# Optimization experiments

Hardware: AMD Instinct MI355X
Metric: run time of the kernel (lower is better)

Reference implementation:

```python
import jax, jax.numpy as jnp
import numpy as np

EMBED_DIM = 1024
NUM_HEADS = 16
HEAD_DIM = EMBED_DIM // NUM_HEADS
B, L = 4, 2048


def setup_inputs() -> dict:
    key = jax.random.key(0)
    k1, k2, k3 = jax.random.split(key, 3)
    s = 1.0 / np.sqrt(EMBED_DIM)
    x = jax.random.normal(k1, (B, L, EMBED_DIM), dtype=jnp.float32)
    w_qkv = jax.random.normal(k2, (EMBED_DIM, 3 * EMBED_DIM), dtype=jnp.float32) * s
    b_qkv = jnp.zeros((3 * EMBED_DIM,), dtype=jnp.float32)
    w_out = jax.random.normal(k3, (EMBED_DIM, EMBED_DIM), dtype=jnp.float32) * s
    b_out = jnp.zeros((EMBED_DIM,), dtype=jnp.float32)
    return {"x": x, "w_qkv": w_qkv, "b_qkv": b_qkv, "w_out": w_out, "b_out": b_out}


def reference(x, w_qkv, b_qkv, w_out, b_out):
    Bb, Ll, _ = x.shape
    scale = HEAD_DIM ** -0.5
    qkv = x @ w_qkv + b_qkv                      # [B, L, 3E]
    qkv = qkv.reshape(Bb, Ll, 3, NUM_HEADS, HEAD_DIM)
    q, k, v = qkv[:, :, 0], qkv[:, :, 1], qkv[:, :, 2]   # [B, L, H, D]
    # scores: [B, H, L, L]
    scores = jnp.einsum("bqhd,bkhd->bhqk", q, k) * scale
    causal = jnp.tril(jnp.ones((Ll, Ll), dtype=bool))     # True = keep
    scores = jnp.where(causal, scores, jnp.float32(-1e9))
    attn_probs = jax.nn.softmax(scores, axis=-1)
    context = jnp.einsum("bhqk,bkhd->bqhd", attn_probs, v)
    context = context.reshape(Bb, Ll, EMBED_DIM)
    out = context @ w_out + b_out
    return (out, attn_probs)
```

## Files before the change

kernel.cpp:

```cpp
#include <hip/hip_runtime.h>


typedef __attribute__((ext_vector_type(8))) short short8;
typedef __attribute__((ext_vector_type(4))) float f32x4;

#define MFMA_BF16(a,b,c) __builtin_amdgcn_mfma_f32_16x16x32_bf16((a),(b),(c),0,0,0)

#define GLDS(gp, lp) __builtin_amdgcn_global_load_lds( \
    (const __attribute__((address_space(1))) unsigned int*)(gp), \
    (__attribute__((address_space(3))) unsigned int*)(lp), 16, 0, 0)

__device__ __forceinline__ unsigned short f2bf(float f) {
    union { float f; unsigned u; } v; v.f = f;
    return (unsigned short)((v.u + 0x7FFFu + ((v.u >> 16) & 1u)) >> 16);
}

#define QK_SCALE 0.18033688011112042f

__global__ __launch_bounds__(256) void k_cast(const float* __restrict__ src,
                                              unsigned short* __restrict__ dst, int n8) {
    int i = blockIdx.x * 256 + threadIdx.x;
    if (i >= n8) return;
    const float4* s = (const float4*)src + (size_t)i * 2;
    float4 a = s[0], b = s[1];
    short8 o;
    o[0] = f2bf(a.x); o[1] = f2bf(a.y); o[2] = f2bf(a.z); o[3] = f2bf(a.w);
    o[4] = f2bf(b.x); o[5] = f2bf(b.y); o[6] = f2bf(b.z); o[7] = f2bf(b.w);
    ((short8*)dst)[i] = o;
}

__global__ __launch_bounds__(256) void k_transpose_cast(const float* __restrict__ src,
                                                        unsigned short* __restrict__ dst,
                                                        int R, int C) {
    __shared__ unsigned short t[64][72];
    int c0 = blockIdx.x * 64, r0 = blockIdx.y * 64;
    int tid = threadIdx.x;
    int rl = tid >> 2, cs = (tid & 3) * 16;
    const float* sp = src + (size_t)(r0 + rl) * C + c0 + cs;
    #pragma unroll
    for (int j = 0; j < 16; j += 4) {
        float4 v = *(const float4*)(sp + j);
        t[rl][cs + j + 0] = f2bf(v.x);
        t[rl][cs + j + 1] = f2bf(v.y);
        t[rl][cs + j + 2] = f2bf(v.z);
        t[rl][cs + j + 3] = f2bf(v.w);
    }
    __syncthreads();
    int clq = tid >> 2, rs = (tid & 3) * 16;
    short8 o0, o1;
    #pragma unroll
    for (int j = 0; j < 8; ++j) o0[j] = (short)t[rs + j][clq];
    #pragma unroll
    for (int j = 0; j < 8; ++j) o1[j] = (short)t[rs + 8 + j][clq];
    unsigned short* dp = dst + (size_t)(c0 + clq) * R + r0 + rs;
    *(short8*)dp = o0;
    *(short8*)(dp + 8) = o1;
}

__global__ __launch_bounds__(256) void k_gemm_qkv(
    const unsigned short* __restrict__ A,
    const unsigned short* __restrict__ Bt,
    const float* __restrict__ bias,
    unsigned short* __restrict__ qb,
    unsigned short* __restrict__ kb,
    unsigned short* __restrict__ vb)
{
    __shared__ unsigned short As[128 * 32];
    __shared__ unsigned short Bs[128 * 32];
    const int m0 = blockIdx.y * 128, n0 = blockIdx.x * 128;
    const int tid = threadIdx.x, w = tid >> 6, l = tid & 63;
    const int wm = w >> 1, wn = w & 1;
    const int g = l >> 4, cl = l & 15;
    const int srow = w * 16 + (l >> 2);
    const int soff = (l & 3) * 8;
    f32x4 acc[4][4] = {};

    for (int k0 = 0; k0 < 1024; k0 += 32) {
        __syncthreads();
        #pragma unroll
        for (int c = 0; c < 2; ++c) {
            GLDS(A  + (size_t)(m0 + c * 64 + srow) * 1024 + k0 + soff, &As[(c * 64 + w * 16) * 32]);
            GLDS(Bt + (size_t)(n0 + c * 64 + srow) * 1024 + k0 + soff, &Bs[(c * 64 + w * 16) * 32]);
        }
        __syncthreads();
        short8 af[4], bfr[4];
        #pragma unroll
        for (int i = 0; i < 4; ++i) af[i]  = *(const short8*)&As[(wm * 64 + i * 16 + cl) * 32 + g * 8];
        #pragma unroll
        for (int i = 0; i < 4; ++i) bfr[i] = *(const short8*)&Bs[(wn * 64 + i * 16 + cl) * 32 + g * 8];
        #pragma unroll
        for (int mi = 0; mi < 4; ++mi)
            #pragma unroll
            for (int ni = 0; ni < 4; ++ni)
                acc[mi][ni] = MFMA_BF16(af[mi], bfr[ni], acc[mi][ni]);
    }
    #pragma unroll
    for (int ni = 0; ni < 4; ++ni) {
        int col = n0 + wn * 64 + ni * 16 + cl;
        int which = col >> 10, h = (col >> 6) & 15, d = col & 63;
        unsigned short* dst = which == 0 ? qb : (which == 1 ? kb : vb);
        float bv = bias[col];
        float sc = (which == 0) ? QK_SCALE : 1.0f;
        #pragma unroll
        for (int mi = 0; mi < 4; ++mi) {
            #pragma unroll
            for (int i = 0; i < 4; ++i) {
                int row = m0 + wm * 64 + mi * 16 + g * 4 + i;
                int b = row >> 11, ll = row & 2047;
                dst[((size_t)(b * 16 + h) * 2048 + ll) * 64 + d] = f2bf((acc[mi][ni][i] + bv) * sc);
            }
        }
    }
}

__global__ __launch_bounds__(256) void k_gemm_out(
    const unsigned short* __restrict__ A,
    const unsigned short* __restrict__ Bt,
    const float* __restrict__ bias,
    float* __restrict__ out)
{
    __shared__ unsigned short As[128 * 32];
    __shared__ unsigned short Bs[128 * 32];
    const int m0 = blockIdx.y * 128, n0 = blockIdx.x * 128;
    const int tid = threadIdx.x, w = tid >> 6, l = tid & 63;
    const int wm = w >> 1, wn = w & 1;
    const int g = l >> 4, cl = l & 15;
    const int srow = w * 16 + (l >> 2);
    const int soff = (l & 3) * 8;
    f32x4 acc[4][4] = {};

    for (int k0 = 0; k0 < 1024; k0 += 32) {
        __syncthreads();
        #pragma unroll
        for (int c = 0; c < 2; ++c) {
            GLDS(A  + (size_t)(m0 + c * 64 + srow) * 1024 + k0 + soff, &As[(c * 64 + w * 16) * 32]);
            GLDS(Bt + (size_t)(n0 + c * 64 + srow) * 1024 + k0 + soff, &Bs[(c * 64 + w * 16) * 32]);
        }
        __syncthreads();
        short8 af[4], bfr[4];
        #pragma unroll
        for (int i = 0; i < 4; ++i) af[i]  = *(const short8*)&As[(wm * 64 + i * 16 + cl) * 32 + g * 8];
        #pragma unroll
        for (int i = 0; i < 4; ++i) bfr[i] = *(const short8*)&Bs[(wn * 64 + i * 16 + cl) * 32 + g * 8];
        #pragma unroll
        for (int mi = 0; mi < 4; ++mi)
            #pragma unroll
            for (int ni = 0; ni < 4; ++ni)
                acc[mi][ni] = MFMA_BF16(af[mi], bfr[ni], acc[mi][ni]);
    }
    #pragma unroll
    for (int ni = 0; ni < 4; ++ni) {
        int col = n0 + wn * 64 + ni * 16 + cl;
        float bv = bias[col];
        #pragma unroll
        for (int mi = 0; mi < 4; ++mi) {
            #pragma unroll
            for (int i = 0; i < 4; ++i) {
                int row = m0 + wm * 64 + mi * 16 + g * 4 + i;
                out[(size_t)row * 1024 + col] = acc[mi][ni][i] + bv;
            }
        }
    }
}

__device__ __forceinline__ void stage_qk(const unsigned short* gbase,
                                         unsigned short* lds, int w, int l) {
    const int lr = l >> 3;
    const int lc = (l & 7) ^ lr;
    #pragma unroll
    for (int c = 0; c < 2; ++c) {
        const int r0 = (w * 2 + c) * 8;
        GLDS(gbase + (size_t)(r0 + lr) * 64 + (lc << 3), lds + r0 * 64);
    }
}

__global__ __launch_bounds__(256, 4) void k_attn(
    const unsigned short* __restrict__ qb,
    const unsigned short* __restrict__ kb,
    const unsigned short* __restrict__ vb,
    float* __restrict__ probs,
    unsigned short* __restrict__ ctx)
{
    __shared__ unsigned short Ks[2][64 * 64];
    __shared__ unsigned short Vt[2][64 * 64];
    __shared__ unsigned short Ps[4 * 16 * 64];

    const int lid = blockIdx.y * 32 + blockIdx.x;
    const int nl  = (lid & 7) * 256 + (lid >> 3);
    const int qt  = 31 - (nl & 31);
    const int bh  = nl >> 5;

    const int tid = threadIdx.x;
    const int w = tid >> 6, l = tid & 63;
    const int g = l >> 4, cl = l & 15;

    const unsigned short* Qg = qb + (size_t)bh * (2048 * 64);
    const unsigned short* Kg = kb + (size_t)bh * (2048 * 64);
    const unsigned short* Vg = vb + (size_t)bh * (2048 * 64);

    stage_qk(Qg + (size_t)qt * (64 * 64), Vt[0], w, l);
    stage_qk(Kg, Ks[0], w, l);
    __syncthreads();

    const int qr = w * 16 + cl;
    short8 aq0 = *(const short8*)&Vt[0][qr * 64 + ((g ^ (qr & 7)) << 3)];
    short8 aq1 = *(const short8*)&Vt[0][qr * 64 + (((g + 4) ^ (qr & 7)) << 3)];

    f32x4 lpart = {0.f, 0.f, 0.f, 0.f};
    for (int kt = 0; kt <= qt; ++kt) {
        const unsigned short* K = Ks[kt & 1];
        if (kt < qt) {
            stage_qk(Kg + (size_t)(kt + 1) * (64 * 64), Ks[(kt & 1) ^ 1], w, l);
            #pragma unroll
            for (int kf = 0; kf < 4; ++kf) {
                int r = kf * 16 + cl;
                short8 b0 = *(const short8*)&K[r * 64 + ((g ^ (r & 7)) << 3)];
                short8 b1 = *(const short8*)&K[r * 64 + (((g + 4) ^ (r & 7)) << 3)];
                f32x4 acc = {0.f, 0.f, 0.f, 0.f};
                acc = MFMA_BF16(aq0, b0, acc);
                acc = MFMA_BF16(aq1, b1, acc);
                #pragma unroll
                for (int i = 0; i < 4; ++i)
                    lpart[i] += __builtin_amdgcn_exp2f(acc[i]);
            }
        } else {
            #pragma unroll
            for (int kf = 0; kf < 4; ++kf) {
                int r = kf * 16 + cl;
                short8 b0 = *(const short8*)&K[r * 64 + ((g ^ (r & 7)) << 3)];
                short8 b1 = *(const short8*)&K[r * 64 + (((g + 4) ^ (r & 7)) << 3)];
                f32x4 acc = {0.f, 0.f, 0.f, 0.f};
                acc = MFMA_BF16(aq0, b0, acc);
                acc = MFMA_BF16(aq1, b1, acc);
                #pragma unroll
                for (int i = 0; i < 4; ++i) {
                    float e = __builtin_amdgcn_exp2f(acc[i]);
                    lpart[i] += (r > w * 16 + g * 4 + i) ? 0.f : e;
                }
            }
        }
        __syncthreads();
    }

    f32x4 lr;
    #pragma unroll
    for (int i = 0; i < 4; ++i) {
        float s = lpart[i];
        s += __shfl_xor(s, 1);
        s += __shfl_xor(s, 2);
        s += __shfl_xor(s, 4);
        s += __shfl_xor(s, 8);
        lr[i] = -__log2f(s);
    }

    stage_qk(Kg, Ks[0], w, l);
    const int vkp = tid & 31;
    const int vd0 = (tid >> 5) * 8;
    short8 va  = *(const short8*)(Vg + (size_t)(2 * vkp) * 64 + vd0);
    short8 vb8 = *(const short8*)(Vg + (size_t)(2 * vkp + 1) * 64 + vd0);

    f32x4 cacc[4] = {};

    for (int kt = 0; kt <= qt; ++kt) {
        const int cur = kt & 1;
        const bool last = (kt == qt);

        unsigned int* VtW = (unsigned int*)Vt[cur];
        #pragma unroll
        for (int j = 0; j < 8; ++j) {
            unsigned int pk = (unsigned int)(unsigned short)va[j]
                            | ((unsigned int)(unsigned short)vb8[j] << 16);
            VtW[(vd0 + j) * 32 + (((vkp >> 2) ^ j) << 2) + (vkp & 3)] = pk;
        }
        if (!last) {
            va  = *(const short8*)(Vg + (size_t)((kt + 1) * 64 + 2 * vkp) * 64 + vd0);
            vb8 = *(const short8*)(Vg + (size_t)((kt + 1) * 64 + 2 * vkp + 1) * 64 + vd0);
        }
        __syncthreads();

        if (!last) stage_qk(Kg + (size_t)(kt + 1) * (64 * 64), Ks[cur ^ 1], w, l);

        const unsigned short* K = Ks[cur];
        size_t prow = ((size_t)bh * 2048 + qt * 64 + w * 16 + g * 4) * 2048 + kt * 64;
        #pragma unroll
        for (int kf = 0; kf < 4; ++kf) {
            int r = kf * 16 + cl;
            short8 b0 = *(const short8*)&K[r * 64 + ((g ^ (r & 7)) << 3)];
            short8 b1 = *(const short8*)&K[r * 64 + (((g + 4) ^ (r & 7)) << 3)];
            f32x4 acc = {0.f, 0.f, 0.f, 0.f};
            acc = MFMA_BF16(aq0, b0, acc);
            acc = MFMA_BF16(aq1, b1, acc);
            #pragma unroll
            for (int i = 0; i < 4; ++i) {
                float p = __builtin_amdgcn_exp2f(acc[i] + lr[i]);
                if (last && r > w * 16 + g * 4 + i) p = 0.f;
                probs[prow + (size_t)i * 2048 + kf * 16 + cl] = p;
                int rr = g * 4 + i;
                int scol = (((2 * kf + (cl >> 3)) ^ (rr & 7)) << 3) + (cl & 7);
                Ps[(w * 16 + rr) * 64 + scol] = f2bf(p);
            }
        }

        #pragma unroll
        for (int kk = 0; kk < 2; ++kk) {
            short8 pa = *(const short8*)&Ps[(w * 16 + cl) * 64 + (((kk * 4 + g) ^ (cl & 7)) << 3)];
            #pragma unroll
            for (int df = 0; df < 4; ++df) {
                int vr = df * 16 + cl;
                short8 vf = *(const short8*)&Vt[cur][vr * 64 + (((kk * 4 + g) ^ (vr & 7)) << 3)];
                cacc[df] = MFMA_BF16(pa, vf, cacc[df]);
            }
        }
    }

    {
        const int b = bh >> 4, h = bh & 15;
        #pragma unroll
        for (int df = 0; df < 4; ++df) {
            #pragma unroll
            for (int i = 0; i < 4; ++i) {
                int row = qt * 64 + w * 16 + g * 4 + i;
                ctx[((size_t)(b * 2048 + row)) * 1024 + h * 64 + df * 16 + cl] = f2bf(cacc[df][i]);
            }
        }
    }

    {
        const int col0 = (qt + 1) * 64;
        if (col0 < 2048) {
            const f32x4 z = {0.f, 0.f, 0.f, 0.f};
            float* tp = probs + ((size_t)bh * 2048 + qt * 64) * 2048;
            for (int r = 0; r < 64; ++r) {
                float* rp = tp + (size_t)r * 2048;
                for (int cc = col0 + tid * 4; cc < 2048; cc += 1024)
                    __builtin_nontemporal_store(z, (f32x4*)&rp[cc]);
            }
        }
    }
}

extern "C" void kernel_launch(void* const* d_in, const int* in_sizes, int n_in,
                              void* d_out, int out_size, void* d_ws, size_t ws_size,
                              hipStream_t stream) {
    const float* x     = (const float*)d_in[0];
    const float* w_qkv = (const float*)d_in[1];
    const float* b_qkv = (const float*)d_in[2];
    const float* w_out = (const float*)d_in[3];
    const float* b_out = (const float*)d_in[4];

    float* out   = (float*)d_out;
    float* probs = out + (size_t)8192 * 1024;

    char* ws = (char*)d_ws;
    unsigned short* xb    = (unsigned short*)(ws);
    unsigned short* wqkvT = (unsigned short*)(ws + 16777216);
    unsigned short* woutT = (unsigned short*)(ws + 23068672);
    unsigned short* qb    = (unsigned short*)(ws + 25165824);
    unsigned short* kb    = (unsigned short*)(ws + 41943040);
    unsigned short* vb    = (unsigned short*)(ws + 58720256);
    unsigned short* ctx   = xb;

    k_cast<<<4096, 256, 0, stream>>>(x, xb, 1048576);
    k_transpose_cast<<<dim3(48, 16), 256, 0, stream>>>(w_qkv, wqkvT, 1024, 3072);
    k_transpose_cast<<<dim3(16, 16), 256, 0, stream>>>(w_out, woutT, 1024, 1024);
    k_gemm_qkv<<<dim3(24, 64), 256, 0, stream>>>(xb, wqkvT, b_qkv, qb, kb, vb);
    k_attn<<<dim3(32, 64), 256, 0, stream>>>(qb, kb, vb, probs, ctx);
    k_gemm_out<<<dim3(8, 64), 256, 0, stream>>>(ctx, woutT, b_out, out);
}
```

Before: 396.4 us.

## Transpose MFMA operand order so each lane holds contiguous columns for vector stores

The QK and PV MFMA calls now pass operands in swapped order, so each lane's four accumulator values run along the key or head dimension rather than across rows. This lets probability rows be written as one 16-byte store per lane, P tiles be written to LDS as packed 8-byte chunks, and context be written as 4-element short vectors, in place of scalar scattered stores. The row-sum reduction shrinks to one scalar per lane with cross-group shuffles. It targets the uncoalesced global writes of the large probs tensor. The risk lies in the swizzle and mask index changes, which must stay consistent with the PV read pattern.

```diff
diff --git a/kernel.cpp b/kernel.cpp
--- a/kernel.cpp
+++ b/kernel.cpp
@@ -2,7 +2,9 @@
 
 
 typedef __attribute__((ext_vector_type(8))) short short8;
+typedef __attribute__((ext_vector_type(4))) short short4v;
 typedef __attribute__((ext_vector_type(4))) float f32x4;
+typedef __attribute__((ext_vector_type(2))) unsigned int u32x2;
 
 #define MFMA_BF16(a,b,c) __builtin_amdgcn_mfma_f32_16x16x32_bf16((a),(b),(c),0,0,0)
 
@@ -206,7 +208,7 @@
     short8 aq0 = *(const short8*)&Vt[0][qr * 64 + ((g ^ (qr & 7)) << 3)];
     short8 aq1 = *(const short8*)&Vt[0][qr * 64 + (((g + 4) ^ (qr & 7)) << 3)];
 
-    f32x4 lpart = {0.f, 0.f, 0.f, 0.f};
+    float lpart = 0.f;
     for (int kt = 0; kt <= qt; ++kt) {
         const unsigned short* K = Ks[kt & 1];
         if (kt < qt) {
@@ -217,11 +219,11 @@
                 short8 b0 = *(const short8*)&K[r * 64 + ((g ^ (r & 7)) << 3)];
                 short8 b1 = *(const short8*)&K[r * 64 + (((g + 4) ^ (r & 7)) << 3)];
                 f32x4 acc = {0.f, 0.f, 0.f, 0.f};
-                acc = MFMA_BF16(aq0, b0, acc);
-                acc = MFMA_BF16(aq1, b1, acc);
+                acc = MFMA_BF16(b0, aq0, acc);
+                acc = MFMA_BF16(b1, aq1, acc);
                 #pragma unroll
                 for (int i = 0; i < 4; ++i)
-                    lpart[i] += __builtin_amdgcn_exp2f(acc[i]);
+                    lpart += __builtin_amdgcn_exp2f(acc[i]);
             }
         } else {
             #pragma unroll
@@ -230,27 +232,24 @@
                 short8 b0 = *(const short8*)&K[r * 64 + ((g ^ (r & 7)) << 3)];
                 short8 b1 = *(const short8*)&K[r * 64 + (((g + 4) ^ (r & 7)) << 3)];
                 f32x4 acc = {0.f, 0.f, 0.f, 0.f};
-                acc = MFMA_BF16(aq0, b0, acc);
-                acc = MFMA_BF16(aq1, b1, acc);
+                acc = MFMA_BF16(b0, aq0, acc);
+                acc = MFMA_BF16(b1, aq1, acc);
                 #pragma unroll
                 for (int i = 0; i < 4; ++i) {
                     float e = __builtin_amdgcn_exp2f(acc[i]);
-                    lpart[i] += (r > w * 16 + g * 4 + i) ? 0.f : e;
+                    lpart += ((kf * 16 + g * 4 + i) > qr) ? 0.f : e;
                 }
             }
         }
         __syncthreads();
     }
 
-    f32x4 lr;
-    #pragma unroll
-    for (int i = 0; i < 4; ++i) {
-        float s = lpart[i];
-        s += __shfl_xor(s, 1);
-        s += __shfl_xor(s, 2);
-        s += __shfl_xor(s, 4);
-        s += __shfl_xor(s, 8);
-        lr[i] = -__log2f(s);
+    float lr;
+    {
+        float s = lpart;
+        s += __shfl_xor(s, 16);
+        s += __shfl_xor(s, 32);
+        lr = -__log2f(s);
     }
 
     stage_qk(Kg, Ks[0], w, l);
@@ -260,6 +259,7 @@
     short8 vb8 = *(const short8*)(Vg + (size_t)(2 * vkp + 1) * 64 + vd0);
 
     f32x4 cacc[4] = {};
+    const size_t prow = ((size_t)bh * 2048 + qt * 64 + qr) * 2048;
 
     for (int kt = 0; kt <= qt; ++kt) {
         const int cur = kt & 1;
@@ -281,47 +281,51 @@
         if (!last) stage_qk(Kg + (size_t)(kt + 1) * (64 * 64), Ks[cur ^ 1], w, l);
 
         const unsigned short* K = Ks[cur];
-        size_t prow = ((size_t)bh * 2048 + qt * 64 + w * 16 + g * 4) * 2048 + kt * 64;
         #pragma unroll
         for (int kf = 0; kf < 4; ++kf) {
             int r = kf * 16 + cl;
             short8 b0 = *(const short8*)&K[r * 64 + ((g ^ (r & 7)) << 3)];
             short8 b1 = *(const short8*)&K[r * 64 + (((g + 4) ^ (r & 7)) << 3)];
             f32x4 acc = {0.f, 0.f, 0.f, 0.f};
-            acc = MFMA_BF16(aq0, b0, acc);
-            acc = MFMA_BF16(aq1, b1, acc);
+            acc = MFMA_BF16(b0, aq0, acc);
+            acc = MFMA_BF16(b1, aq1, acc);
+            f32x4 p4;
             #pragma unroll
             for (int i = 0; i < 4; ++i) {
-                float p = __builtin_amdgcn_exp2f(acc[i] + lr[i]);
-                if (last && r > w * 16 + g * 4 + i) p = 0.f;
-                probs[prow + (size_t)i * 2048 + kf * 16 + cl] = p;
-                int rr = g * 4 + i;
-                int scol = (((2 * kf + (cl >> 3)) ^ (rr & 7)) << 3) + (cl & 7);
-                Ps[(w * 16 + rr) * 64 + scol] = f2bf(p);
-            }
-        }
-
-        #pragma unroll
-        for (int kk = 0; kk < 2; ++kk) {
-            short8 pa = *(const short8*)&Ps[(w * 16 + cl) * 64 + (((kk * 4 + g) ^ (cl & 7)) << 3)];
+                float p = __builtin_amdgcn_exp2f(acc[i] + lr);
+                if (last && (kf * 16 + g * 4 + i) > qr) p = 0.f;
+                p4[i] = p;
+            }
+            *(f32x4*)&probs[prow + kt * 64 + kf * 16 + g * 4] = p4;
+            u32x2 uq;
+            uq[0] = (unsigned)f2bf(p4[0]) | ((unsigned)f2bf(p4[1]) << 16);
+            uq[1] = (unsigned)f2bf(p4[2]) | ((unsigned)f2bf(p4[3]) << 16);
+            int e0 = (kf * 16 + g * 4) ^ ((cl & 7) << 3);
+            *(u32x2*)&Ps[(w * 16 + cl) * 64 + e0] = uq;
+        }
+
+        #pragma unroll
+        for (int ks = 0; ks < 2; ++ks) {
+            int er = (ks * 32 + g * 8) ^ ((cl & 7) << 3);
+            short8 paf = *(const short8*)&Ps[(w * 16 + cl) * 64 + er];
             #pragma unroll
             for (int df = 0; df < 4; ++df) {
                 int vr = df * 16 + cl;
-                short8 vf = *(const short8*)&Vt[cur][vr * 64 + (((kk * 4 + g) ^ (vr & 7)) << 3)];
-                cacc[df] = MFMA_BF16(pa, vf, cacc[df]);
+                short8 vf = *(const short8*)&Vt[cur][vr * 64 + (((ks * 4 + g) ^ (vr & 7)) << 3)];
+                cacc[df] = MFMA_BF16(vf, paf, cacc[df]);
             }
         }
     }
 
     {
         const int b = bh >> 4, h = bh & 15;
+        const size_t crow = ((size_t)(b * 2048 + qt * 64 + qr)) * 1024 + h * 64;
         #pragma unroll
         for (int df = 0; df < 4; ++df) {
-            #pragma unroll
-            for (int i = 0; i < 4; ++i) {
-                int row = qt * 64 + w * 16 + g * 4 + i;
-                ctx[((size_t)(b * 2048 + row)) * 1024 + h * 64 + df * 16 + cl] = f2bf(cacc[df][i]);
-            }
+            short4v cv;
+            #pragma unroll
+            for (int i = 0; i < 4; ++i) cv[i] = (short)f2bf(cacc[df][i]);
+            *(short4v*)&ctx[crow + df * 16 + g * 4] = cv;
         }
     }
 
```

Result: faster. 388.0 us (-2.1%).
